# Optimization experiments

Measured on AMD Instinct MI355X. Metric: run time of the kernel, lower is better.

The kernel has to match this reference:

```python
import jax, jax.numpy as jnp
import numpy as np

WINDOW = 7
HEADS = 8


def setup_inputs() -> dict:
    key = jax.random.key(0)
    ks = jax.random.split(key, 6)
    B, L, C = 4096, WINDOW * WINDOW, 256
    x = jax.random.normal(ks[0], (B, L, C), dtype=jnp.float32)
    relative_index = jax.random.randint(ks[1], (L * L,), 0, (2 * WINDOW - 1) ** 2, dtype=jnp.int32)
    qkv_w = jax.random.normal(ks[2], (C, 3 * C), dtype=jnp.float32) * 0.02
    qkv_b = jnp.zeros((3 * C,), dtype=jnp.float32)
    rel_bias = jax.random.normal(ks[3], ((2 * WINDOW - 1) ** 2, HEADS), dtype=jnp.float32) * 0.02
    proj_w = jax.random.normal(ks[4], (C, C), dtype=jnp.float32) * 0.02
    proj_b = jnp.zeros((C,), dtype=jnp.float32)
    return {"x": x, "relative_index": relative_index, "qkv_w": qkv_w, "qkv_b": qkv_b,
            "rel_bias": rel_bias, "proj_w": proj_w, "proj_b": proj_b}


def reference(x, relative_index, qkv_w, qkv_b, rel_bias, proj_w, proj_b):
    B, L, C = x.shape
    H = HEADS
    D = C // H
    scale = D ** -0.5
    # qkv projection -> [3, B, H, L, D]
    qkv = (x @ qkv_w + qkv_b).reshape(B, L, 3, H, D).transpose(2, 0, 3, 1, 4)
    q, k, v = qkv[0], qkv[1], qkv[2]
    attn = jnp.einsum('bhld,bhmd->bhlm', q * scale, k)  # [B,H,L,L]
    # gather relative position bias: [L*L, H] -> [H, L, L]
    bias = rel_bias[relative_index].reshape(L, L, H).transpose(2, 0, 1)
    attn = jax.nn.softmax(attn + bias[None], axis=-1)
    out = jnp.einsum('bhlm,bhmd->blhd', attn, v).reshape(B, L, C)
    return out @ proj_w + proj_b
```

## Files before the change

kernel.cpp:

```cpp
#include <hip/hip_runtime.h>


typedef short s8v __attribute__((ext_vector_type(8)));
typedef short s4v __attribute__((ext_vector_type(4)));
typedef float f4  __attribute__((ext_vector_type(4)));

#define MFMA(a,b,c) __builtin_amdgcn_mfma_f32_16x16x32_bf16((a),(b),(c),0,0,0)

__device__ __forceinline__ unsigned short f2bf(float f) {
    unsigned u = __float_as_uint(f);
    u = u + 0x7fffu + ((u >> 16) & 1u);
    return (unsigned short)(u >> 16);
}

__device__ __forceinline__ unsigned pkbf(float lo, float hi) {
    unsigned r;
    asm("v_cvt_pk_bf16_f32 %0, %1, %2" : "=v"(r) : "v"(lo), "v"(hi));
    return r;
}

__global__ void prep(const float* __restrict__ qkv_w, const float* __restrict__ proj_w,
                     const float* __restrict__ rel_bias, const int* __restrict__ rel_idx,
                     unsigned short* __restrict__ wq, unsigned short* __restrict__ wp,
                     float* __restrict__ biasT2)
{
    int idx = blockIdx.x * blockDim.x + threadIdx.x;
    int stride = gridDim.x * blockDim.x;
    for (int i = idx; i < 48*8*64*8; i += stride) {
        int j = i & 7, l = (i >> 3) & 63, ks = (i >> 9) & 7, nt = i >> 12;
        int k = ks*32 + (l >> 4)*8 + j;
        int n = nt*16 + (l & 15);
        wq[i] = f2bf(qkv_w[k*768 + n]);
    }
    for (int i = idx; i < 16*8*64*8; i += stride) {
        int j = i & 7, l = (i >> 3) & 63, ks = (i >> 9) & 7, nt = i >> 12;
        int k = ks*32 + (l >> 4)*8 + j;
        int n = nt*16 + (l & 15);
        wp[i] = f2bf(proj_w[k*256 + n]);
    }
    for (int i = idx; i < 8*64*64; i += stride) {
        int k = i & 63, q = (i >> 6) & 63, h = i >> 12;
        float v;
        if (k < 49) v = (q < 49) ? rel_bias[rel_idx[q*49 + k]*8 + h] : 0.f;
        else        v = -1e30f;
        biasT2[i] = v;
    }
}

__global__ __launch_bounds__(512, 2) void kall(
    const float* __restrict__ x, const float* __restrict__ qkv_b,
    const unsigned short* __restrict__ wq, const float* __restrict__ biasT2,
    const unsigned short* __restrict__ wp, const float* __restrict__ proj_b,
    float* __restrict__ out)
{
    __shared__ __align__(16) unsigned short xs[4][8][64][8];
    __shared__ __align__(16) unsigned short osd[64][264];

    const int b    = blockIdx.x;
    const int tid  = threadIdx.x;
    const int w    = tid >> 6;
    const int lane = tid & 63;
    const int ln   = lane & 15;
    const int g    = lane >> 4;

    const float* xb = x + (size_t)b * (49*256);
    for (int i = tid; i < 4096; i += 512) {
        int r = i >> 6, c4 = i & 63;
        float4 v = make_float4(0.f, 0.f, 0.f, 0.f);
        if (r < 49) v = ((const float4*)xb)[r*64 + c4];
        uint2 o;
        o.x = pkbf(v.x, v.y);
        o.y = pkbf(v.z, v.w);
        int mt = r >> 4, lnr = r & 15;
        int c  = c4 * 4;
        int ks = c >> 5, gg = (c >> 3) & 3, j0 = c & 7;
        *(uint2*)&xs[mt][ks][(gg*16 + lnr) ^ ks][j0] = o;
    }
    __syncthreads();

    const float scale = 0.17677669529663687f;
    const int h = w;

    f4 qa[2][4], ka[2][4], va[4][2];
    #pragma unroll
    for (int dh = 0; dh < 2; ++dh)
        #pragma unroll
        for (int mt = 0; mt < 4; ++mt) {
            qa[dh][mt] = (f4){0.f,0.f,0.f,0.f};
            ka[dh][mt] = (f4){0.f,0.f,0.f,0.f};
            va[mt][dh] = (f4){0.f,0.f,0.f,0.f};
        }

    #pragma unroll
    for (int ks = 0; ks < 8; ++ks) {
        s8v xf[4];
        #pragma unroll
        for (int mt = 0; mt < 4; ++mt)
            xf[mt] = *(const s8v*)&xs[mt][ks][lane ^ ks][0];
        s8v wfq[2], wfk[2], wfv[2];
        #pragma unroll
        for (int dh = 0; dh < 2; ++dh) {
            wfq[dh] = *(const s8v*)&wq[(size_t)((( 2*h+dh)*8 + ks)*64 + lane) * 8];
            wfk[dh] = *(const s8v*)&wq[(size_t)(((16+2*h+dh)*8 + ks)*64 + lane) * 8];
            wfv[dh] = *(const s8v*)&wq[(size_t)(((32+2*h+dh)*8 + ks)*64 + lane) * 8];
        }
        #pragma unroll
        for (int dh = 0; dh < 2; ++dh)
            #pragma unroll
            for (int mt = 0; mt < 4; ++mt) {
                qa[dh][mt] = MFMA(wfq[dh], xf[mt], qa[dh][mt]);
                ka[dh][mt] = MFMA(wfk[dh], xf[mt], ka[dh][mt]);
                va[mt][dh] = MFMA(xf[mt], wfv[dh], va[mt][dh]);
            }
    }

    float4 bq[2], bk[2]; float bv[2];
    #pragma unroll
    for (int dh = 0; dh < 2; ++dh) {
        bq[dh] = *(const float4*)&qkv_b[       h*32 + dh*16 + g*4];
        bk[dh] = *(const float4*)&qkv_b[256 +  h*32 + dh*16 + g*4];
        bv[dh] = qkv_b[512 + h*32 + dh*16 + ln];
    }

    s8v qf[4], kf[4], vf[2][2];
    #pragma unroll
    for (int t = 0; t < 4; ++t) {
        union { s8v s; unsigned u[4]; } qu, ku;
        qu.u[0] = pkbf((qa[0][t][0] + bq[0].x)*scale, (qa[0][t][1] + bq[0].y)*scale);
        qu.u[1] = pkbf((qa[0][t][2] + bq[0].z)*scale, (qa[0][t][3] + bq[0].w)*scale);
        qu.u[2] = pkbf((qa[1][t][0] + bq[1].x)*scale, (qa[1][t][1] + bq[1].y)*scale);
        qu.u[3] = pkbf((qa[1][t][2] + bq[1].z)*scale, (qa[1][t][3] + bq[1].w)*scale);
        ku.u[0] = pkbf( ka[0][t][0] + bk[0].x,  ka[0][t][1] + bk[0].y);
        ku.u[1] = pkbf( ka[0][t][2] + bk[0].z,  ka[0][t][3] + bk[0].w);
        ku.u[2] = pkbf( ka[1][t][0] + bk[1].x,  ka[1][t][1] + bk[1].y);
        ku.u[3] = pkbf( ka[1][t][2] + bk[1].z,  ka[1][t][3] + bk[1].w);
        qf[t] = qu.s;
        kf[t] = ku.s;
    }
    #pragma unroll
    for (int ksp = 0; ksp < 2; ++ksp)
        #pragma unroll
        for (int dh = 0; dh < 2; ++dh) {
            union { s8v s; unsigned u[4]; } vu;
            vu.u[0] = pkbf(va[2*ksp  ][dh][0] + bv[dh], va[2*ksp  ][dh][1] + bv[dh]);
            vu.u[1] = pkbf(va[2*ksp  ][dh][2] + bv[dh], va[2*ksp  ][dh][3] + bv[dh]);
            vu.u[2] = pkbf(va[2*ksp+1][dh][0] + bv[dh], va[2*ksp+1][dh][1] + bv[dh]);
            vu.u[3] = pkbf(va[2*ksp+1][dh][2] + bv[dh], va[2*ksp+1][dh][3] + bv[dh]);
            vf[ksp][dh] = vu.s;
        }

    #pragma unroll
    for (int qt = 0; qt < 4; ++qt) {
        f4 bias4[4];
        #pragma unroll
        for (int kt = 0; kt < 4; ++kt)
            bias4[kt] = *(const f4*)&biasT2[(size_t)(h*64 + qt*16 + ln)*64 + kt*16 + g*4];

        f4 st[4];
        #pragma unroll
        for (int kt = 0; kt < 4; ++kt) {
            f4 z = (f4){0.f,0.f,0.f,0.f};
            st[kt] = MFMA(kf[kt], qf[qt], z);
        }

        float pr[16];
        float sum = 0.f;
        #pragma unroll
        for (int kt = 0; kt < 4; ++kt)
            #pragma unroll
            for (int r = 0; r < 4; ++r) {
                float e = __expf(st[kt][r] + bias4[kt][r]);
                pr[kt*4 + r] = e;
                sum += e;
            }
        sum += __shfl_xor(sum, 16);
        sum += __shfl_xor(sum, 32);
        float rinv = 1.f / sum;

        s8v pa[2];
        #pragma unroll
        for (int ksp = 0; ksp < 2; ++ksp) {
            union { s8v s; unsigned u[4]; } pu;
            #pragma unroll
            for (int i2 = 0; i2 < 4; ++i2)
                pu.u[i2] = pkbf(pr[8*ksp + 2*i2] * rinv, pr[8*ksp + 2*i2 + 1] * rinv);
            pa[ksp] = pu.s;
        }

        f4 oacc[2];
        oacc[0] = (f4){0.f,0.f,0.f,0.f};
        oacc[1] = (f4){0.f,0.f,0.f,0.f};
        #pragma unroll
        for (int ksp = 0; ksp < 2; ++ksp)
            #pragma unroll
            for (int dh = 0; dh < 2; ++dh)
                oacc[dh] = MFMA(pa[ksp], vf[ksp][dh], oacc[dh]);

        #pragma unroll
        for (int dh = 0; dh < 2; ++dh)
            #pragma unroll
            for (int r = 0; r < 4; ++r)
                osd[qt*16 + g*4 + r][h*32 + dh*16 + ln] = f2bf(oacc[dh][r]);
    }
    __syncthreads();

    f4 acc[4][2];
    #pragma unroll
    for (int mt = 0; mt < 4; ++mt)
        #pragma unroll
        for (int t = 0; t < 2; ++t)
            acc[mt][t] = (f4){0.f,0.f,0.f,0.f};

    #pragma unroll
    for (int ks = 0; ks < 8; ++ks) {
        s8v av[4], bw[2];
        #pragma unroll
        for (int mt = 0; mt < 4; ++mt)
            av[mt] = *(const s8v*)&osd[mt*16 + ln][ks*32 + g*8];
        #pragma unroll
        for (int t = 0; t < 2; ++t) {
            int nt = w*2 + t;
            bw[t] = *(const s8v*)&wp[(size_t)((nt*8 + ks)*64 + lane) * 8];
        }
        #pragma unroll
        for (int mt = 0; mt < 4; ++mt)
            #pragma unroll
            for (int t = 0; t < 2; ++t)
                acc[mt][t] = MFMA(av[mt], bw[t], acc[mt][t]);
    }

    float* ob = out + (size_t)b * (49*256);
    #pragma unroll
    for (int t = 0; t < 2; ++t) {
        int n = (w*2 + t)*16 + ln;
        float pb = proj_b[n];
        #pragma unroll
        for (int mt = 0; mt < 4; ++mt)
            #pragma unroll
            for (int r = 0; r < 4; ++r) {
                int q = mt*16 + g*4 + r;
                if (q < 49)
                    ob[q*256 + n] = acc[mt][t][r] + pb;
            }
    }
}

extern "C" void kernel_launch(void* const* d_in, const int* in_sizes, int n_in,
                              void* d_out, int out_size, void* d_ws, size_t ws_size,
                              hipStream_t stream)
{
    (void)n_in; (void)out_size; (void)ws_size;
    const float* x        = (const float*)d_in[0];
    const int*   rel_idx  = (const int*)  d_in[1];
    const float* qkv_w    = (const float*)d_in[2];
    const float* qkv_b    = (const float*)d_in[3];
    const float* rel_bias = (const float*)d_in[4];
    const float* proj_w   = (const float*)d_in[5];
    const float* proj_b   = (const float*)d_in[6];
    float* out = (float*)d_out;

    const int B = in_sizes[0] / (49*256);

    unsigned short* wq = (unsigned short*)d_ws;
    unsigned short* wp = wq + 48*8*64*8;
    float* biasT2 = (float*)((char*)d_ws + 524288);

    prep<<<256, 256, 0, stream>>>(qkv_w, proj_w, rel_bias, rel_idx, wq, wp, biasT2);
    kall<<<B, 512, 0, stream>>>(x, qkv_b, wq, biasT2, wp, proj_b, out);
}
```

Baseline: 295.7 us.

## Split QKV projection loops to cut live accumulators and raise occupancy

Restructures the QKV projection so Q/K accumulators are computed one M-tile at a time and V in two M-tile pairs, instead of holding all 32 accumulators live at once. Raises launch bounds from 2 to 4 blocks per CU to exploit the lower register pressure. The cost is reloading the weight fragments from global memory several times (once per M-tile loop) and re-reading x from LDS, trading extra loads for higher occupancy. LDS usage of about 66KB per block may also limit the achievable 4 blocks per CU.

```diff
diff --git a/kernel.cpp b/kernel.cpp
--- a/kernel.cpp
+++ b/kernel.cpp
@@ -47,7 +47,7 @@
     }
 }
 
-__global__ __launch_bounds__(512, 2) void kall(
+__global__ __launch_bounds__(512, 4) void kall(
     const float* __restrict__ x, const float* __restrict__ qkv_b,
     const unsigned short* __restrict__ wq, const float* __restrict__ biasT2,
     const unsigned short* __restrict__ wp, const float* __restrict__ proj_b,
@@ -81,39 +81,6 @@
     const float scale = 0.17677669529663687f;
     const int h = w;
 
-    f4 qa[2][4], ka[2][4], va[4][2];
-    #pragma unroll
-    for (int dh = 0; dh < 2; ++dh)
-        #pragma unroll
-        for (int mt = 0; mt < 4; ++mt) {
-            qa[dh][mt] = (f4){0.f,0.f,0.f,0.f};
-            ka[dh][mt] = (f4){0.f,0.f,0.f,0.f};
-            va[mt][dh] = (f4){0.f,0.f,0.f,0.f};
-        }
-
-    #pragma unroll
-    for (int ks = 0; ks < 8; ++ks) {
-        s8v xf[4];
-        #pragma unroll
-        for (int mt = 0; mt < 4; ++mt)
-            xf[mt] = *(const s8v*)&xs[mt][ks][lane ^ ks][0];
-        s8v wfq[2], wfk[2], wfv[2];
-        #pragma unroll
-        for (int dh = 0; dh < 2; ++dh) {
-            wfq[dh] = *(const s8v*)&wq[(size_t)((( 2*h+dh)*8 + ks)*64 + lane) * 8];
-            wfk[dh] = *(const s8v*)&wq[(size_t)(((16+2*h+dh)*8 + ks)*64 + lane) * 8];
-            wfv[dh] = *(const s8v*)&wq[(size_t)(((32+2*h+dh)*8 + ks)*64 + lane) * 8];
-        }
-        #pragma unroll
-        for (int dh = 0; dh < 2; ++dh)
-            #pragma unroll
-            for (int mt = 0; mt < 4; ++mt) {
-                qa[dh][mt] = MFMA(wfq[dh], xf[mt], qa[dh][mt]);
-                ka[dh][mt] = MFMA(wfk[dh], xf[mt], ka[dh][mt]);
-                va[mt][dh] = MFMA(xf[mt], wfv[dh], va[mt][dh]);
-            }
-    }
-
     float4 bq[2], bk[2]; float bv[2];
     #pragma unroll
     for (int dh = 0; dh < 2; ++dh) {
@@ -123,31 +90,72 @@
     }
 
     s8v qf[4], kf[4], vf[2][2];
-    #pragma unroll
-    for (int t = 0; t < 4; ++t) {
+
+    #pragma unroll
+    for (int mt = 0; mt < 4; ++mt) {
+        f4 qa[2], ka[2];
+        qa[0] = (f4){0.f,0.f,0.f,0.f}; qa[1] = (f4){0.f,0.f,0.f,0.f};
+        ka[0] = (f4){0.f,0.f,0.f,0.f}; ka[1] = (f4){0.f,0.f,0.f,0.f};
+        #pragma unroll
+        for (int ks = 0; ks < 8; ++ks) {
+            s8v xf = *(const s8v*)&xs[mt][ks][lane ^ ks][0];
+            s8v wfq[2], wfk[2];
+            #pragma unroll
+            for (int dh = 0; dh < 2; ++dh) {
+                wfq[dh] = *(const s8v*)&wq[(size_t)((( 2*h+dh)*8 + ks)*64 + lane) * 8];
+                wfk[dh] = *(const s8v*)&wq[(size_t)(((16+2*h+dh)*8 + ks)*64 + lane) * 8];
+            }
+            #pragma unroll
+            for (int dh = 0; dh < 2; ++dh) {
+                qa[dh] = MFMA(wfq[dh], xf, qa[dh]);
+                ka[dh] = MFMA(wfk[dh], xf, ka[dh]);
+            }
+        }
         union { s8v s; unsigned u[4]; } qu, ku;
-        qu.u[0] = pkbf((qa[0][t][0] + bq[0].x)*scale, (qa[0][t][1] + bq[0].y)*scale);
-        qu.u[1] = pkbf((qa[0][t][2] + bq[0].z)*scale, (qa[0][t][3] + bq[0].w)*scale);
-        qu.u[2] = pkbf((qa[1][t][0] + bq[1].x)*scale, (qa[1][t][1] + bq[1].y)*scale);
-        qu.u[3] = pkbf((qa[1][t][2] + bq[1].z)*scale, (qa[1][t][3] + bq[1].w)*scale);
-        ku.u[0] = pkbf( ka[0][t][0] + bk[0].x,  ka[0][t][1] + bk[0].y);
-        ku.u[1] = pkbf( ka[0][t][2] + bk[0].z,  ka[0][t][3] + bk[0].w);
-        ku.u[2] = pkbf( ka[1][t][0] + bk[1].x,  ka[1][t][1] + bk[1].y);
-        ku.u[3] = pkbf( ka[1][t][2] + bk[1].z,  ka[1][t][3] + bk[1].w);
-        qf[t] = qu.s;
-        kf[t] = ku.s;
-    }
-    #pragma unroll
-    for (int ksp = 0; ksp < 2; ++ksp)
+        qu.u[0] = pkbf((qa[0][0] + bq[0].x)*scale, (qa[0][1] + bq[0].y)*scale);
+        qu.u[1] = pkbf((qa[0][2] + bq[0].z)*scale, (qa[0][3] + bq[0].w)*scale);
+        qu.u[2] = pkbf((qa[1][0] + bq[1].x)*scale, (qa[1][1] + bq[1].y)*scale);
+        qu.u[3] = pkbf((qa[1][2] + bq[1].z)*scale, (qa[1][3] + bq[1].w)*scale);
+        ku.u[0] = pkbf( ka[0][0] + bk[0].x,  ka[0][1] + bk[0].y);
+        ku.u[1] = pkbf( ka[0][2] + bk[0].z,  ka[0][3] + bk[0].w);
+        ku.u[2] = pkbf( ka[1][0] + bk[1].x,  ka[1][1] + bk[1].y);
+        ku.u[3] = pkbf( ka[1][2] + bk[1].z,  ka[1][3] + bk[1].w);
+        qf[mt] = qu.s;
+        kf[mt] = ku.s;
+    }
+
+    #pragma unroll
+    for (int msp = 0; msp < 2; ++msp) {
+        f4 va[2][2];
+        #pragma unroll
+        for (int mtl = 0; mtl < 2; ++mtl) {
+            va[mtl][0] = (f4){0.f,0.f,0.f,0.f};
+            va[mtl][1] = (f4){0.f,0.f,0.f,0.f};
+        }
+        #pragma unroll
+        for (int ks = 0; ks < 8; ++ks) {
+            s8v xf0 = *(const s8v*)&xs[2*msp  ][ks][lane ^ ks][0];
+            s8v xf1 = *(const s8v*)&xs[2*msp+1][ks][lane ^ ks][0];
+            s8v wfv[2];
+            #pragma unroll
+            for (int dh = 0; dh < 2; ++dh)
+                wfv[dh] = *(const s8v*)&wq[(size_t)(((32+2*h+dh)*8 + ks)*64 + lane) * 8];
+            #pragma unroll
+            for (int dh = 0; dh < 2; ++dh) {
+                va[0][dh] = MFMA(xf0, wfv[dh], va[0][dh]);
+                va[1][dh] = MFMA(xf1, wfv[dh], va[1][dh]);
+            }
+        }
         #pragma unroll
         for (int dh = 0; dh < 2; ++dh) {
             union { s8v s; unsigned u[4]; } vu;
-            vu.u[0] = pkbf(va[2*ksp  ][dh][0] + bv[dh], va[2*ksp  ][dh][1] + bv[dh]);
-            vu.u[1] = pkbf(va[2*ksp  ][dh][2] + bv[dh], va[2*ksp  ][dh][3] + bv[dh]);
-            vu.u[2] = pkbf(va[2*ksp+1][dh][0] + bv[dh], va[2*ksp+1][dh][1] + bv[dh]);
-            vu.u[3] = pkbf(va[2*ksp+1][dh][2] + bv[dh], va[2*ksp+1][dh][3] + bv[dh]);
-            vf[ksp][dh] = vu.s;
-        }
+            vu.u[0] = pkbf(va[0][dh][0] + bv[dh], va[0][dh][1] + bv[dh]);
+            vu.u[1] = pkbf(va[0][dh][2] + bv[dh], va[0][dh][3] + bv[dh]);
+            vu.u[2] = pkbf(va[1][dh][0] + bv[dh], va[1][dh][1] + bv[dh]);
+            vu.u[3] = pkbf(va[1][dh][2] + bv[dh], va[1][dh][3] + bv[dh]);
+            vf[msp][dh] = vu.s;
+        }
+    }
 
     #pragma unroll
     for (int qt = 0; qt < 4; ++qt) {
```

Result: slower. 553.3 us (+87.2%).
